# Optimization experiments

Hardware: AMD Instinct MI355X
Metric: run time of the kernel (lower is better)

## Reference

```python
import jax, jax.numpy as jnp
import numpy as np

B, N, M = 2, 1024, 512
D, H, DH = 1024, 16, 64          # features, heads, head dim (D == H*DH)
MID = H * DH
DC = 768                          # context_features
MULT = 4
EPS = 1e-5


def _ln(x, w, b):
    mu = jnp.mean(x, -1, keepdims=True)
    var = jnp.mean((x - mu) ** 2, -1, keepdims=True)
    return (x - mu) * jax.lax.rsqrt(var + EPS) * w + b


def _sincos(n, d):
    inv = 1.0 / (10000.0 ** (jnp.arange(0, d, 2, dtype=jnp.float32) / d))
    ang = jnp.arange(n, dtype=jnp.float32)[:, None] * inv[None, :]
    return jnp.sin(ang), jnp.cos(ang)


def _rope(x, sin, cos):
    # x: [B,H,N,DH]; sin/cos: [N, DH//2]; interleaved even/odd rotation
    s = sin[None, None]
    c = cos[None, None]
    xe = x[..., ::2]
    xo = x[..., 1::2]
    re = xe * c - xo * s
    ro = xe * s + xo * c
    return jnp.stack((re, ro), axis=-1).reshape(x.shape)


def _heads(t):
    b, n, _ = t.shape
    return t.reshape(b, n, H, DH).transpose(0, 2, 1, 3)


def _attn(xq, ctx, wq, wkv, wo, bo):
    q = _heads(xq @ wq)
    k, v = jnp.split(ctx @ wkv, 2, axis=-1)
    k = _heads(k)
    v = _heads(v)
    sq, cq = _sincos(q.shape[2], DH)
    sk, ck = _sincos(k.shape[2], DH)
    q = _rope(q, sq, cq)
    k = _rope(k, sk, ck)
    sim = jnp.einsum('bhnd,bhmd->bhnm', q, k) * (DH ** -0.5)
    a = jax.nn.softmax(sim, axis=-1)
    o = jnp.einsum('bhnm,bhmd->bhnd', a, v)
    o = o.transpose(0, 2, 1, 3).reshape(xq.shape[0], xq.shape[1], MID)
    return o @ wo + bo


def _adaln(x, c, lw, lb, gw, gb, bw, bb):
    g = (c @ gw + gb)[:, None, :]
    bt = (c @ bw + bb)[:, None, :]
    return _ln(x, lw, lb) * (1.0 + g) + bt


def setup_inputs() -> dict:
    ks = jax.random.split(jax.random.key(0), 24)
    s = 0.02
    inp = {
        'x': jax.random.normal(ks[0], (B, N, D), jnp.float32),
        'cond': jax.random.normal(ks[1], (B, D), jnp.float32),
        'context': jax.random.normal(ks[2], (B, M, DC), jnp.float32),
        # AdaLN (attn_mod) — reused for self- and cross-attention pre-norm
        'ln1_w': jnp.ones((D,), jnp.float32),
        'ln1_b': jnp.zeros((D,), jnp.float32),
        'g1_w': jax.random.normal(ks[3], (D, D), jnp.float32) * s,
        'g1_b': jnp.zeros((D,), jnp.float32),
        'b1_w': jax.random.normal(ks[4], (D, D), jnp.float32) * s,
        'b1_b': jnp.zeros((D,), jnp.float32),
        # AdaLN (ffn_mod)
        'ln2_w': jnp.ones((D,), jnp.float32),
        'ln2_b': jnp.zeros((D,), jnp.float32),
        'g2_w': jax.random.normal(ks[5], (D, D), jnp.float32) * s,
        'g2_b': jnp.zeros((D,), jnp.float32),
        'b2_w': jax.random.normal(ks[6], (D, D), jnp.float32) * s,
        'b2_b': jnp.zeros((D,), jnp.float32),
        # self-attention
        'sa_wq': jax.random.normal(ks[7], (D, MID), jnp.float32) * s,
        'sa_wkv': jax.random.normal(ks[8], (D, 2 * MID), jnp.float32) * s,
        'sa_wo': jax.random.normal(ks[9], (MID, D), jnp.float32) * s,
        'sa_bo': jnp.zeros((D,), jnp.float32),
        # cross-attention (context LayerNorm + projections)
        'ca_lnc_w': jnp.ones((DC,), jnp.float32),
        'ca_lnc_b': jnp.zeros((DC,), jnp.float32),
        'ca_wq': jax.random.normal(ks[10], (D, MID), jnp.float32) * s,
        'ca_wkv': jax.random.normal(ks[11], (DC, 2 * MID), jnp.float32) * s,
        'ca_wo': jax.random.normal(ks[12], (MID, D), jnp.float32) * s,
        'ca_bo': jnp.zeros((D,), jnp.float32),
        # FFN
        'ff_w1': jax.random.normal(ks[13], (D, MULT * D), jnp.float32) * s,
        'ff_b1': jnp.zeros((MULT * D,), jnp.float32),
        'ff_w2': jax.random.normal(ks[14], (MULT * D, D), jnp.float32) * s,
        'ff_b2': jnp.zeros((D,), jnp.float32),
    }
    return inp


def reference(x, cond, context,
              ln1_w, ln1_b, g1_w, g1_b, b1_w, b1_b,
              ln2_w, ln2_b, g2_w, g2_b, b2_w, b2_b,
              sa_wq, sa_wkv, sa_wo, sa_bo,
              ca_lnc_w, ca_lnc_b, ca_wq, ca_wkv, ca_wo, ca_bo,
              ff_w1, ff_b1, ff_w2, ff_b2):
    # self-attention with shared attn_mod AdaLN
    attn_in = _adaln(x, cond, ln1_w, ln1_b, g1_w, g1_b, b1_w, b1_b)
    x = _attn(attn_in, attn_in, sa_wq, sa_wkv, sa_wo, sa_bo) + x
    # cross-attention (attn_mod reused, context LayerNorm applied)
    cross_in = _adaln(x, cond, ln1_w, ln1_b, g1_w, g1_b, b1_w, b1_b)
    ctx_n = _ln(context, ca_lnc_w, ca_lnc_b)
    x = _attn(cross_in, ctx_n, ca_wq, ca_wkv, ca_wo, ca_bo) + x
    # FFN with ffn_mod AdaLN, exact GELU (torch default)
    ffn_in = _adaln(x, cond, ln2_w, ln2_b, g2_w, g2_b, b2_w, b2_b)
    h = jax.nn.gelu(ffn_in @ ff_w1 + ff_b1, approximate=False)
    x = h @ ff_w2 + ff_b2 + x
    return x
```

## Files before the change

kernel.cpp:

```cpp
#include <hip/hip_runtime.h>
#include <hip/hip_bf16.h>
#include <math.h>


typedef float f32x4 __attribute__((ext_vector_type(4)));
typedef __bf16 bf16x8 __attribute__((ext_vector_type(8)));
typedef __bf16 bf16x4 __attribute__((ext_vector_type(4)));
typedef __bf16 bf16x2 __attribute__((ext_vector_type(2)));

#define DEVI __device__ __forceinline__

DEVI void gload16(const void* g, void* l) {
  __builtin_amdgcn_global_load_lds((const __attribute__((address_space(1))) void*)g,
                                   (__attribute__((address_space(3))) void*)l, 16, 0, 0);
}

DEVI float fast_gelu(float x) {
  float a = fabsf(x) * 0.7071067811865475f;
  float tt = 1.0f / (1.0f + 0.3275911f * a);
  float p = tt * (0.254829592f + tt * (-0.284496736f + tt * (1.421413741f +
            tt * (-1.453152027f + tt * 1.061405429f))));
  float er = 1.0f - p * __expf(-a * a);
  er = (x < 0.f) ? -er : er;
  return 0.5f * x * (1.0f + er);
}

struct WtDesc {
  const float* src[8];
  __bf16* dst[8];
  int K[8], N[8];
  int tstart[9];
};

__global__ __launch_bounds__(256) void prep_kernel(WtDesc d,
                                                   float2* __restrict__ tbl,
                                                   const float* __restrict__ cond,
                                                   const float* __restrict__ g1w,
                                                   const float* __restrict__ b1w,
                                                   const float* __restrict__ g2w,
                                                   const float* __restrict__ b2w,
                                                   float* __restrict__ part) {
  __shared__ float smem[32][33];
  int blk = blockIdx.x;
  int wtend = d.tstart[8];
  if (blk < wtend) {
    int e = 0;
#pragma unroll
    for (int i = 0; i < 7; ++i) e += (blk >= d.tstart[i + 1]) ? 1 : 0;
    int li = blk - d.tstart[e];
    const float* W = d.src[e];
    __bf16* WT = d.dst[e];
    int K = d.K[e], N = d.N[e];
    int ntx = N >> 5;
    int n0 = (li % ntx) * 32, k0 = (li / ntx) * 32;
    int tx = threadIdx.x & 31, ty = threadIdx.x >> 5;
#pragma unroll
    for (int i = 0; i < 4; ++i) {
      int k = ty + i * 8;
      smem[k][tx] = W[(size_t)(k0 + k) * N + n0 + tx];
    }
    __syncthreads();
#pragma unroll
    for (int i = 0; i < 4; ++i) {
      int n = ty + i * 8;
      WT[(size_t)(n0 + n) * K + k0 + tx] = (__bf16)smem[tx][n];
    }
  } else if (blk < wtend + 128) {
    int idx = (blk - wtend) * 256 + threadIdx.x;
    int n = idx >> 5, i = idx & 31;
    float inv = expf(-(float)(2 * i) * (1.0f / 64.0f) * 9.210340371976184f);
    float ang = (float)n * inv;
    tbl[idx] = make_float2(sinf(ang), cosf(ang));
  } else {
    int f = blk - wtend - 128;
    int dchunk = f & 3, b = (f >> 2) & 1, z = f >> 3;
    int mat = z >> 3, ks = z & 7;
    const float* W = (mat == 0) ? g1w : (mat == 1) ? b1w : (mat == 2) ? g2w : b2w;
    float* sc = &smem[0][0];
    if (threadIdx.x < 128) sc[threadIdx.x] = cond[b * 1024 + ks * 128 + threadIdx.x];
    __syncthreads();
    int dd = dchunk * 256 + threadIdx.x;
    const float* Wp = W + (size_t)(ks * 128) * 1024 + dd;
    float acc = 0.f;
#pragma unroll 8
    for (int k = 0; k < 128; ++k) acc += sc[k] * Wp[(size_t)k * 1024];
    part[(size_t)(z * 2 + b) * 1024 + dd] = acc;
  }
}

__global__ __launch_bounds__(256) void mod_reduce_kernel(
    const float* __restrict__ part,
    const float* __restrict__ g1b, const float* __restrict__ b1b,
    const float* __restrict__ g2b, const float* __restrict__ b2b,
    float* __restrict__ mods) {
  int idx = blockIdx.x * 256 + threadIdx.x;
  int mat = idx >> 11, b = (idx >> 10) & 1, d = idx & 1023;
  float s = 0.f;
#pragma unroll
  for (int ks = 0; ks < 8; ++ks) s += part[(size_t)((mat * 8 + ks) * 2 + b) * 1024 + d];
  const float* Bv = (mat == 0) ? g1b : (mat == 1) ? b1b : (mat == 2) ? g2b : b2b;
  mods[(size_t)(mat * 2 + b) * 1024 + d] = s + Bv[d];
}

__global__ __launch_bounds__(256) void adaln_kernel(const float* __restrict__ X,
                                                    const float* __restrict__ lnw,
                                                    const float* __restrict__ lnb,
                                                    const float* __restrict__ mods,
                                                    int gi, int bi,
                                                    __bf16* __restrict__ out) {
  __shared__ float red[2][4];
  int row = blockIdx.x;
  int b = row >> 10;
  int t = threadIdx.x;
  const float4 xv = ((const float4*)(X + (size_t)row * 1024))[t];
  float s  = xv.x + xv.y + xv.z + xv.w;
  float s2 = xv.x * xv.x + xv.y * xv.y + xv.z * xv.z + xv.w * xv.w;
  int lane = t & 63, w = t >> 6;
#pragma unroll
  for (int off = 32; off > 0; off >>= 1) {
    s += __shfl_down(s, off);
    s2 += __shfl_down(s2, off);
  }
  if (lane == 0) { red[0][w] = s; red[1][w] = s2; }
  __syncthreads();
  s  = red[0][0] + red[0][1] + red[0][2] + red[0][3];
  s2 = red[1][0] + red[1][1] + red[1][2] + red[1][3];
  float mu = s * (1.0f / 1024.0f);
  float var = s2 * (1.0f / 1024.0f) - mu * mu;
  float rstd = rsqrtf(var + 1e-5f);
  const float4 wv = ((const float4*)lnw)[t];
  const float4 bv = ((const float4*)lnb)[t];
  const float4 gv = ((const float4*)(mods + (size_t)(gi * 2 + b) * 1024))[t];
  const float4 tv = ((const float4*)(mods + (size_t)(bi * 2 + b) * 1024))[t];
  bf16x4 ov;
  ov[0] = (__bf16)(((xv.x - mu) * rstd * wv.x + bv.x) * (1.0f + gv.x) + tv.x);
  ov[1] = (__bf16)(((xv.y - mu) * rstd * wv.y + bv.y) * (1.0f + gv.y) + tv.y);
  ov[2] = (__bf16)(((xv.z - mu) * rstd * wv.z + bv.z) * (1.0f + gv.z) + tv.z);
  ov[3] = (__bf16)(((xv.w - mu) * rstd * wv.w + bv.w) * (1.0f + gv.w) + tv.w);
  *(bf16x4*)(out + (size_t)row * 1024 + t * 4) = ov;
}

__global__ __launch_bounds__(256) void ctxln_kernel(const float* __restrict__ X,
                                                    const float* __restrict__ w,
                                                    const float* __restrict__ bias,
                                                    __bf16* __restrict__ out) {
  __shared__ float red[2][4];
  int row = blockIdx.x;
  int t = threadIdx.x;
  const float* xp = X + (size_t)row * 768;
  float v[3];
  float s = 0.f, s2 = 0.f;
#pragma unroll
  for (int i = 0; i < 3; ++i) {
    v[i] = xp[t + i * 256];
    s += v[i];
    s2 += v[i] * v[i];
  }
  int lane = t & 63, wv_ = t >> 6;
#pragma unroll
  for (int off = 32; off > 0; off >>= 1) {
    s += __shfl_down(s, off);
    s2 += __shfl_down(s2, off);
  }
  if (lane == 0) { red[0][wv_] = s; red[1][wv_] = s2; }
  __syncthreads();
  s  = red[0][0] + red[0][1] + red[0][2] + red[0][3];
  s2 = red[1][0] + red[1][1] + red[1][2] + red[1][3];
  float mu = s * (1.0f / 768.0f);
  float var = s2 * (1.0f / 768.0f) - mu * mu;
  float rstd = rsqrtf(var + 1e-5f);
#pragma unroll
  for (int i = 0; i < 3; ++i) {
    int c = t + i * 256;
    out[(size_t)row * 768 + c] = (__bf16)((v[i] - mu) * rstd * w[c] + bias[c]);
  }
}

__global__ __launch_bounds__(256) void vtb_kernel(const __bf16* __restrict__ Vb,
                                                  __bf16* __restrict__ VT, int Ntok) {
  __shared__ __bf16 tile[64][68];
  int bh = blockIdx.x, nt = blockIdx.y;
  int b = bh >> 4, h = bh & 15;
  int t = threadIdx.x;
  int tx = t & 15, ty = t >> 4;
#pragma unroll
  for (int i = 0; i < 4; ++i) {
    int n = ty + i * 16;
    bf16x4 v = *(const bf16x4*)(Vb + (size_t)(b * Ntok + nt * 64 + n) * 1024 + h * 64 + tx * 4);
#pragma unroll
    for (int j = 0; j < 4; ++j) tile[n][tx * 4 + j] = v[j];
  }
  __syncthreads();
#pragma unroll
  for (int i = 0; i < 4; ++i) {
    int d = ty + i * 16;
    bf16x4 o;
#pragma unroll
    for (int j = 0; j < 4; ++j) o[j] = tile[tx * 4 + j][d];
    *(bf16x4*)(VT + ((size_t)bh * 64 + d) * Ntok + nt * 64 + tx * 4) = o;
  }
}

template <int BM, int BN, int EPI, int DEPTH>
__global__ __launch_bounds__(256) void gemm3(const __bf16* __restrict__ A,
                                             const __bf16* __restrict__ BT,
                                             const float* __restrict__ bias,
                                             const float* __restrict__ res,
                                             void* __restrict__ outv,
                                             int M, int N, int K, int kslices,
                                             const float2* __restrict__ tbl,
                                             __bf16* __restrict__ Qro,
                                             __bf16* __restrict__ Kro,
                                             __bf16* __restrict__ Vbo,
                                             int Ntok) {
  constexpr int MI = BM / 32, NI = BN / 32;
  constexpr int NBUF = DEPTH + 1;
  constexpr int LPT = BM / 64 + BN / 64;
  __shared__ __bf16 sA[NBUF][BM * 32];
  __shared__ __bf16 sB[NBUF][BN * 32];
  const int t = threadIdx.x;
  const int w = t >> 6, lane = t & 63;
  const int lr = lane & 15, lg = lane >> 4;
  const int fxor = (lr >> 1) & 3;
  int nwg = gridDim.x * gridDim.y * gridDim.z;
  int flat = blockIdx.x + gridDim.x * (blockIdx.y + gridDim.y * blockIdx.z);
  flat = (flat & 7) * (nwg >> 3) + (flat >> 3);
  const int bm = flat % gridDim.x;
  int rest = flat / gridDim.x;
  const int bn = rest % gridDim.y;
  const int bz = rest / gridDim.y;
  const int wm = (w >> 1) * (BM / 2), wn = (w & 1) * (BN / 2);
  const int kper = K / kslices;
  const int k0 = bz * kper;
  const int nsteps = kper / 32;
  f32x4 acc[MI][NI] = {};

  auto stage = [&](int buf, int kt) {
#pragma unroll
    for (int i = 0; i < BM / 64; ++i) {
      int e8 = i * 256 + t;
      int row = e8 >> 2, c = e8 & 3;
      int scol = (c ^ ((row >> 1) & 3)) << 3;
      gload16(A + (size_t)(bm * BM + row) * K + kt + scol, &sA[buf][e8 * 8]);
    }
#pragma unroll
    for (int i = 0; i < BN / 64; ++i) {
      int e8 = i * 256 + t;
      int row = e8 >> 2, c = e8 & 3;
      int scol = (c ^ ((row >> 1) & 3)) << 3;
      gload16(BT + (size_t)(bn * BN + row) * K + kt + scol, &sB[buf][e8 * 8]);
    }
  };

  auto compute = [&](int buf) {
    bf16x8 af[MI], bfr[NI];
#pragma unroll
    for (int mi = 0; mi < MI; ++mi)
      af[mi] = *(const bf16x8*)(&sA[buf][(wm + mi * 16 + lr) * 32 + ((lg ^ fxor) << 3)]);
#pragma unroll
    for (int ni = 0; ni < NI; ++ni)
      bfr[ni] = *(const bf16x8*)(&sB[buf][(wn + ni * 16 + lr) * 32 + ((lg ^ fxor) << 3)]);
#pragma unroll
    for (int mi = 0; mi < MI; ++mi)
#pragma unroll
      for (int ni = 0; ni < NI; ++ni)
        acc[mi][ni] = __builtin_amdgcn_mfma_f32_16x16x32_bf16(af[mi], bfr[ni], acc[mi][ni], 0, 0, 0);
  };

#pragma unroll
  for (int i = 0; i < DEPTH; ++i) stage(i, k0 + i * 32);

  int it = 0;
  for (; it < nsteps - (DEPTH - 1); ++it) {
    asm volatile("s_waitcnt vmcnt(%0)" :: "n"((DEPTH - 1) * LPT) : "memory");
    __builtin_amdgcn_s_barrier();
    __builtin_amdgcn_sched_barrier(0);
    if (it + DEPTH < nsteps) stage((it + DEPTH) % NBUF, k0 + (it + DEPTH) * 32);
    compute(it % NBUF);
  }
  asm volatile("s_waitcnt vmcnt(0)" ::: "memory");
  __builtin_amdgcn_s_barrier();
  __builtin_amdgcn_sched_barrier(0);
  for (; it < nsteps; ++it) compute(it % NBUF);

#pragma unroll
  for (int mi = 0; mi < MI; ++mi) {
    int row = bm * BM + wm + mi * 16 + lg * 4;
#pragma unroll
    for (int ni = 0; ni < NI; ++ni) {
      int col = bn * BN + wn + ni * 16 + lr;
#pragma unroll
      for (int r = 0; r < 4; ++r) {
        float v = acc[mi][ni][r];
        int erow = row + r;
        size_t off = (size_t)erow * N + col;
        if (EPI == 0) {
          ((float*)outv)[off] = v;
        } else if (EPI == 1) {
          ((float*)outv)[off] = v + bias[col] + res[off];
        } else if (EPI == 2) {
          ((__bf16*)outv)[off] = (__bf16)fast_gelu(v + bias[col]);
        } else if (EPI == 3) {
          ((float*)outv)[(size_t)bz * M * N + off] = v;
        } else if (EPI == 4) {
          float ov = __shfl_xor(v, 1);
          int b = erow >> 10, n = erow & 1023;
          if (col < 2048) {
            int h = (col >> 6) & 15, dh = col & 63;
            float2 sc = tbl[n * 32 + (dh >> 1)];
            float rv = (lr & 1) ? (ov * sc.x + v * sc.y) : (v * sc.y - ov * sc.x);
            __bf16* dst;
            if (col < 1024) { rv *= 0.125f; dst = Qro; } else dst = Kro;
            dst[((size_t)(b * 16 + h) * Ntok + n) * 64 + dh] = (__bf16)rv;
          } else {
            Vbo[(size_t)erow * 1024 + (col - 2048)] = (__bf16)v;
          }
        }
      }
    }
  }
}

__global__ __launch_bounds__(256) void gemm_cross(const __bf16* __restrict__ Aq,
                                                  const __bf16* __restrict__ Bq,
                                                  const __bf16* __restrict__ Akv,
                                                  const __bf16* __restrict__ Bkv,
                                                  const float2* __restrict__ tbl,
                                                  __bf16* __restrict__ Qro,
                                                  __bf16* __restrict__ Kro,
                                                  __bf16* __restrict__ Vbo) {
  constexpr int BM = 128, BN = 64, DEPTH = 3, NBUF = 4, LPT = 3;
  constexpr int MI = 4, NI = 2;
  __shared__ __bf16 sA[NBUF][BM * 32];
  __shared__ __bf16 sB[NBUF][BN * 32];
  const int t = threadIdx.x;
  const int w = t >> 6, lane = t & 63;
  const int lr = lane & 15, lg = lane >> 4;
  const int fxor = (lr >> 1) & 3;
  int flat = blockIdx.x;
  flat = (flat & 7) * 64 + (flat >> 3);
  const bool isq = flat < 256;
  const __bf16* A  = isq ? Aq : Akv;
  const __bf16* BT = isq ? Bq : Bkv;
  const int K = isq ? 1024 : 768;
  int lf = isq ? flat : flat - 256;
  const int bm = isq ? (lf & 15) : (lf & 7);
  const int bn = isq ? (lf >> 4) : (lf >> 3);
  const int wm = (w >> 1) * 64, wn = (w & 1) * 32;
  const int nsteps = K >> 5;
  f32x4 acc[MI][NI] = {};

  auto stage = [&](int buf, int kt) {
#pragma unroll
    for (int i = 0; i < 2; ++i) {
      int e8 = i * 256 + t;
      int row = e8 >> 2, c = e8 & 3;
      int scol = (c ^ ((row >> 1) & 3)) << 3;
      gload16(A + (size_t)(bm * BM + row) * K + kt + scol, &sA[buf][e8 * 8]);
    }
    {
      int e8 = t;
      int row = e8 >> 2, c = e8 & 3;
      int scol = (c ^ ((row >> 1) & 3)) << 3;
      gload16(BT + (size_t)(bn * BN + row) * K + kt + scol, &sB[buf][e8 * 8]);
    }
  };

  auto compute = [&](int buf) {
    bf16x8 af[MI], bfr[NI];
#pragma unroll
    for (int mi = 0; mi < MI; ++mi)
      af[mi] = *(const bf16x8*)(&sA[buf][(wm + mi * 16 + lr) * 32 + ((lg ^ fxor) << 3)]);
#pragma unroll
    for (int ni = 0; ni < NI; ++ni)
      bfr[ni] = *(const bf16x8*)(&sB[buf][(wn + ni * 16 + lr) * 32 + ((lg ^ fxor) << 3)]);
#pragma unroll
    for (int mi = 0; mi < MI; ++mi)
#pragma unroll
      for (int ni = 0; ni < NI; ++ni)
        acc[mi][ni] = __builtin_amdgcn_mfma_f32_16x16x32_bf16(af[mi], bfr[ni], acc[mi][ni], 0, 0, 0);
  };

#pragma unroll
  for (int i = 0; i < DEPTH; ++i) stage(i, i * 32);

  int it = 0;
  for (; it < nsteps - (DEPTH - 1); ++it) {
    asm volatile("s_waitcnt vmcnt(%0)" :: "n"((DEPTH - 1) * LPT) : "memory");
    __builtin_amdgcn_s_barrier();
    __builtin_amdgcn_sched_barrier(0);
    if (it + DEPTH < nsteps) stage((it + DEPTH) % NBUF, (it + DEPTH) * 32);
    compute(it % NBUF);
  }
  asm volatile("s_waitcnt vmcnt(0)" ::: "memory");
  __builtin_amdgcn_s_barrier();
  __builtin_amdgcn_sched_barrier(0);
  for (; it < nsteps; ++it) compute(it % NBUF);

#pragma unroll
  for (int mi = 0; mi < MI; ++mi) {
    int row = bm * 128 + wm + mi * 16 + lg * 4;
#pragma unroll
    for (int ni = 0; ni < NI; ++ni) {
      int col = bn * 64 + wn + ni * 16 + lr;
#pragma unroll
      for (int r = 0; r < 4; ++r) {
        float v = acc[mi][ni][r];
        int erow = row + r;
        float ov = __shfl_xor(v, 1);
        if (isq) {
          int b = erow >> 10, n = erow & 1023;
          int h = col >> 6, dh = col & 63;
          float2 sc = tbl[n * 32 + (dh >> 1)];
          float rv = ((lr & 1) ? (ov * sc.x + v * sc.y) : (v * sc.y - ov * sc.x)) * 0.125f;
          Qro[((size_t)(b * 16 + h) * 1024 + n) * 64 + dh] = (__bf16)rv;
        } else {
          int b = erow >> 9, n = erow & 511;
          if (col < 1024) {
            int h = col >> 6, dh = col & 63;
            float2 sc = tbl[n * 32 + (dh >> 1)];
            float rv = (lr & 1) ? (ov * sc.x + v * sc.y) : (v * sc.y - ov * sc.x);
            Kro[((size_t)(b * 16 + h) * 512 + n) * 64 + dh] = (__bf16)rv;
          } else {
            Vbo[(size_t)erow * 1024 + (col - 1024)] = (__bf16)v;
          }
        }
      }
    }
  }
}

__global__ __launch_bounds__(256) void ff2red_kernel(const float* __restrict__ part,
                                                     const float* __restrict__ bias,
                                                     const float* __restrict__ res,
                                                     float* __restrict__ out, int MN, int N) {
  int idx = blockIdx.x * 256 + threadIdx.x;
  float4 p0 = ((const float4*)part)[idx];
  float4 p1 = ((const float4*)(part + MN))[idx];
  float4 rr = ((const float4*)res)[idx];
  int colb = (idx * 4) & (N - 1);
  float4 bb = *(const float4*)(bias + colb);
  float4 o;
  o.x = p0.x + p1.x + bb.x + rr.x;
  o.y = p0.y + p1.y + bb.y + rr.y;
  o.z = p0.z + p1.z + bb.z + rr.z;
  o.w = p0.w + p1.w + bb.w + rr.w;
  ((float4*)out)[idx] = o;
}

template <int KITERS>
__global__ __launch_bounds__(256) void attn_kernel(const __bf16* __restrict__ Qr,
                                                   const __bf16* __restrict__ Kr,
                                                   const __bf16* __restrict__ VT,
                                                   __bf16* __restrict__ O,
                                                   int Nq, int Nk) {
  __shared__ __bf16 sK[2][64 * 64];
  __shared__ __bf16 sV[2][64 * 64];
  __shared__ __bf16 Pl[4][16 * 64];
  const int t = threadIdx.x, w = t >> 6, lane = t & 63;
  const int lr = lane & 15, lg = lane >> 4;
  const int lsrc = lane & 48;
  const int swz = (lr & 7) << 3;
  int flat = blockIdx.x + (blockIdx.y << 4);
  flat = (flat & 7) * 64 + (flat >> 3);
  const int bh = flat >> 4;
  const int q0 = (flat & 15) * 64 + w * 16;
  const int b = bh >> 4, h = bh & 15;

  auto stage = [&](int buf, int kt) {
#pragma unroll
    for (int i = 0; i < 2; ++i) {
      int e8 = i * 256 + t;
      int row = e8 >> 3, col8 = e8 & 7;
      int scol = (col8 ^ (row & 7)) << 3;
      gload16(Kr + ((size_t)bh * Nk + kt + row) * 64 + scol, &sK[buf][e8 * 8]);
      gload16(VT + ((size_t)bh * 64 + row) * Nk + kt + scol, &sV[buf][e8 * 8]);
    }
  };

  bf16x8 qf[2];
#pragma unroll
  for (int kh = 0; kh < 2; ++kh)
    qf[kh] = *(const bf16x8*)(Qr + ((size_t)bh * Nq + q0 + lr) * 64 + kh * 32 + lg * 8);
  f32x4 accO[4] = {};
  float m = -INFINITY, l = 0.f;

  stage(0, 0);
  __syncthreads();
  int cur = 0;
#pragma unroll
  for (int it = 0; it < KITERS; ++it) {
    if (it + 1 < KITERS) stage(cur ^ 1, (it + 1) * 64);
    f32x4 s[4] = {};
#pragma unroll
    for (int nf = 0; nf < 4; ++nf) {
      int r = nf * 16 + lr;
#pragma unroll
      for (int kh = 0; kh < 2; ++kh) {
        bf16x8 kf = *(const bf16x8*)(&sK[cur][r * 64 + (((kh * 4 + lg) ^ (lr & 7)) << 3)]);
        s[nf] = __builtin_amdgcn_mfma_f32_16x16x32_bf16(kf, qf[kh], s[nf], 0, 0, 0);
      }
    }
    float p[16];
#pragma unroll
    for (int j = 0; j < 16; ++j) p[j] = s[j >> 2][j & 3];
    float pm = p[0];
#pragma unroll
    for (int j = 1; j < 16; ++j) pm = fmaxf(pm, p[j]);
    pm = fmaxf(pm, __shfl_xor(pm, 16));
    pm = fmaxf(pm, __shfl_xor(pm, 32));
    if (!__all(pm <= m + 8.f)) {
      float mnew = fmaxf(m, pm);
      float resc = __expf(m - mnew);
      float rq[4];
#pragma unroll
      for (int r = 0; r < 4; ++r) rq[r] = __shfl(resc, lsrc | (lg * 4 + r));
#pragma unroll
      for (int df = 0; df < 4; ++df)
#pragma unroll
        for (int r = 0; r < 4; ++r) accO[df][r] *= rq[r];
      l *= resc;
      m = mnew;
    }
    float rs = 0.f;
#pragma unroll
    for (int j = 0; j < 16; ++j) { p[j] = __expf(p[j] - m); rs += p[j]; }
    rs += __shfl_xor(rs, 16);
    rs += __shfl_xor(rs, 32);
    l += rs;
#pragma unroll
    for (int nf = 0; nf < 4; ++nf)
#pragma unroll
      for (int jj = 0; jj < 2; ++jj) {
        int k = nf * 16 + lg * 4 + 2 * jj;
        bf16x2 pk;
        pk[0] = (__bf16)p[nf * 4 + 2 * jj];
        pk[1] = (__bf16)p[nf * 4 + 2 * jj + 1];
        *(bf16x2*)(&Pl[w][lr * 64 + (k ^ swz)]) = pk;
      }
    bf16x8 pa0 = *(const bf16x8*)(&Pl[w][lr * 64 + ((lg * 8) ^ swz)]);
    bf16x8 pa1 = *(const bf16x8*)(&Pl[w][lr * 64 + ((32 + lg * 8) ^ swz)]);
#pragma unroll
    for (int df = 0; df < 4; ++df) {
      int d = df * 16 + lr;
      bf16x8 vf0 = *(const bf16x8*)(&sV[cur][d * 64 + ((lg ^ (lr & 7)) << 3)]);
      bf16x8 vf1 = *(const bf16x8*)(&sV[cur][d * 64 + (((4 + lg) ^ (lr & 7)) << 3)]);
      accO[df] = __builtin_amdgcn_mfma_f32_16x16x32_bf16(pa0, vf0, accO[df], 0, 0, 0);
      accO[df] = __builtin_amdgcn_mfma_f32_16x16x32_bf16(pa1, vf1, accO[df], 0, 0, 0);
    }
    __syncthreads();
    cur ^= 1;
  }
  float lq[4];
#pragma unroll
  for (int r = 0; r < 4; ++r) lq[r] = __shfl(l, lsrc | (lg * 4 + r));
#pragma unroll
  for (int r = 0; r < 4; ++r) {
    float inv = 1.0f / lq[r];
    int n = q0 + lg * 4 + r;
#pragma unroll
    for (int df = 0; df < 4; ++df)
      O[(size_t)(b * 1024 + n) * 1024 + h * 64 + df * 16 + lr] = (__bf16)(accO[df][r] * inv);
  }
}

extern "C" void kernel_launch(void* const* d_in, const int* in_sizes, int n_in,
                              void* d_out, int out_size, void* d_ws, size_t ws_size,
                              hipStream_t stream) {
  (void)in_sizes; (void)n_in; (void)out_size; (void)ws_size;
  const float* x       = (const float*)d_in[0];
  const float* cond    = (const float*)d_in[1];
  const float* ctx     = (const float*)d_in[2];
  const float* ln1_w   = (const float*)d_in[3];
  const float* ln1_b   = (const float*)d_in[4];
  const float* g1_w    = (const float*)d_in[5];
  const float* g1_b    = (const float*)d_in[6];
  const float* b1_w    = (const float*)d_in[7];
  const float* b1_b    = (const float*)d_in[8];
  const float* ln2_w   = (const float*)d_in[9];
  const float* ln2_b   = (const float*)d_in[10];
  const float* g2_w    = (const float*)d_in[11];
  const float* g2_b    = (const float*)d_in[12];
  const float* b2_w    = (const float*)d_in[13];
  const float* b2_b    = (const float*)d_in[14];
  const float* sa_wq   = (const float*)d_in[15];
  const float* sa_wkv  = (const float*)d_in[16];
  const float* sa_wo   = (const float*)d_in[17];
  const float* sa_bo   = (const float*)d_in[18];
  const float* ca_lnc_w = (const float*)d_in[19];
  const float* ca_lnc_b = (const float*)d_in[20];
  const float* ca_wq   = (const float*)d_in[21];
  const float* ca_wkv  = (const float*)d_in[22];
  const float* ca_wo   = (const float*)d_in[23];
  const float* ca_bo   = (const float*)d_in[24];
  const float* ff_w1   = (const float*)d_in[25];
  const float* ff_b1   = (const float*)d_in[26];
  const float* ff_w2   = (const float*)d_in[27];
  const float* ff_b2   = (const float*)d_in[28];
  float* out = (float*)d_out;

  char* ws = (char*)d_ws;
  size_t o = 0;
  auto alloc = [&](size_t bytes) {
    void* p = ws + o;
    o += (bytes + 255) & ~(size_t)255;
    return p;
  };

  __bf16* wqT   = (__bf16*)alloc(1024ull * 1024 * 2);
  __bf16* wkvT  = (__bf16*)alloc(2048ull * 1024 * 2);
  __bf16* woT   = (__bf16*)alloc(1024ull * 1024 * 2);
  __bf16* cwqT  = (__bf16*)alloc(1024ull * 1024 * 2);
  __bf16* cwkvT = (__bf16*)alloc(2048ull * 768 * 2);
  __bf16* cwoT  = (__bf16*)alloc(1024ull * 1024 * 2);
  __bf16* ff1T  = (__bf16*)alloc(4096ull * 1024 * 2);
  __bf16* ff2T  = (__bf16*)alloc(1024ull * 4096 * 2);
  float*  mods  = (float*)alloc(4ull * 2 * 1024 * 4);
  float2* tbl   = (float2*)alloc(1024ull * 32 * 8);
  __bf16* ain   = (__bf16*)alloc(2048ull * 1024 * 2);
  float*  Qf    = (float*)alloc(2048ull * 1024 * 4);
  float*  KVf   = (float*)alloc(2048ull * 2048 * 4);
  __bf16* ctxn  = (__bf16*)alloc(1024ull * 768 * 2);
  __bf16* Qr    = (__bf16*)alloc(2048ull * 1024 * 2);
  __bf16* Kr    = (__bf16*)alloc(2048ull * 1024 * 2);
  __bf16* VTb   = (__bf16*)alloc(2048ull * 1024 * 2);
  __bf16* Ob    = (__bf16*)alloc(2048ull * 1024 * 2);
  float*  x1    = (float*)alloc(2048ull * 1024 * 4);
  float*  x2    = (float*)alloc(2048ull * 1024 * 4);
  __bf16* hb    = (__bf16*)KVf;
  float*  pbuf  = (float*)Qr;
  float*  wopb  = (float*)KVf;
  float*  mpart = (float*)Qf;
  __bf16* Vb    = (__bf16*)Qf;

  WtDesc wd;
  const float* srcs[8] = {sa_wq, sa_wkv, sa_wo, ca_wq, ca_wkv, ca_wo, ff_w1, ff_w2};
  __bf16* dsts[8] = {wqT, wkvT, woT, cwqT, cwkvT, cwoT, ff1T, ff2T};
  int Ks[8] = {1024, 1024, 1024, 1024, 768, 1024, 1024, 4096};
  int Ns[8] = {1024, 2048, 1024, 1024, 2048, 1024, 4096, 1024};
  int cum = 0;
  for (int i = 0; i < 8; ++i) {
    wd.src[i] = srcs[i]; wd.dst[i] = dsts[i]; wd.K[i] = Ks[i]; wd.N[i] = Ns[i];
    wd.tstart[i] = cum;
    cum += (Ks[i] >> 5) * (Ns[i] >> 5);
  }
  wd.tstart[8] = cum;
  prep_kernel<<<cum + 128 + 256, 256, 0, stream>>>(wd, tbl, cond, g1_w, b1_w, g2_w, b2_w, mpart);
  mod_reduce_kernel<<<32, 256, 0, stream>>>(mpart, g1_b, b1_b, g2_b, b2_b, mods);

  adaln_kernel<<<2048, 256, 0, stream>>>(x, ln1_w, ln1_b, mods, 0, 1, ain);
  gemm3<128, 64, 4, 3><<<dim3(16, 48), 256, 0, stream>>>(ain, wqT, nullptr, nullptr, nullptr,
                                                         2048, 3072, 1024, 1, tbl, Qr, Kr, Vb, 1024);
  vtb_kernel<<<dim3(32, 16), 256, 0, stream>>>(Vb, VTb, 1024);
  attn_kernel<16><<<dim3(16, 32), 256, 0, stream>>>(Qr, Kr, VTb, Ob, 1024, 1024);
  gemm3<128, 64, 3, 3><<<dim3(16, 16, 2), 256, 0, stream>>>(Ob, woT, nullptr, nullptr, wopb,
                                                            2048, 1024, 1024, 2, nullptr, nullptr, nullptr, nullptr, 0);
  ff2red_kernel<<<2048, 256, 0, stream>>>(wopb, sa_bo, x, x1, 2048 * 1024, 1024);

  adaln_kernel<<<2048, 256, 0, stream>>>(x1, ln1_w, ln1_b, mods, 0, 1, ain);
  ctxln_kernel<<<1024, 256, 0, stream>>>(ctx, ca_lnc_w, ca_lnc_b, ctxn);
  gemm_cross<<<512, 256, 0, stream>>>(ain, cwqT, ctxn, cwkvT, tbl, Qr, Kr, Vb);
  vtb_kernel<<<dim3(32, 8), 256, 0, stream>>>(Vb, VTb, 512);
  attn_kernel<8><<<dim3(16, 32), 256, 0, stream>>>(Qr, Kr, VTb, Ob, 1024, 512);
  gemm3<128, 64, 3, 3><<<dim3(16, 16, 2), 256, 0, stream>>>(Ob, cwoT, nullptr, nullptr, wopb,
                                                            2048, 1024, 1024, 2, nullptr, nullptr, nullptr, nullptr, 0);
  ff2red_kernel<<<2048, 256, 0, stream>>>(wopb, ca_bo, x1, x2, 2048 * 1024, 1024);

  adaln_kernel<<<2048, 256, 0, stream>>>(x2, ln2_w, ln2_b, mods, 2, 3, ain);
  gemm3<128, 128, 2, 2><<<dim3(16, 32), 256, 0, stream>>>(ain, ff1T, ff_b1, nullptr, hb,
                                                          2048, 4096, 1024, 1, nullptr, nullptr, nullptr, nullptr, 0);
  gemm3<128, 64, 3, 3><<<dim3(16, 16, 2), 256, 0, stream>>>(hb, ff2T, nullptr, nullptr, pbuf,
                                                            2048, 1024, 4096, 2, nullptr, nullptr, nullptr, nullptr, 0);
  ff2red_kernel<<<2048, 256, 0, stream>>>(pbuf, ff_b2, x2, out, 2048 * 1024, 1024);
}
```

Baseline: 246.4 us.

## Fuse split-K reduction with AdaLN and widen weight-transpose tiles

Replaces the split-K reduce plus residual kernel followed by a separate AdaLN kernel with one kernel. The fused kernel sums the partials, adds bias and residual, writes the new residual stream, then applies LayerNorm and modulation from registers, so the residual is not read back from memory. The weight transpose/bf16 conversion in the prep kernel now handles 32x128 tiles with float4 loads and 16-byte bf16x8 stores, which cuts the block count and uses wider memory transactions. Both changes save memory traffic and launches, at the cost of more LDS per prep block.

```diff
diff --git a/kernel.cpp b/kernel.cpp
--- a/kernel.cpp
+++ b/kernel.cpp
@@ -40,9 +40,10 @@
                                                    const float* __restrict__ g2w,
                                                    const float* __restrict__ b2w,
                                                    float* __restrict__ part) {
-  __shared__ float smem[32][33];
+  __shared__ float smem[32 * 129];
   int blk = blockIdx.x;
   int wtend = d.tstart[8];
+  int t = threadIdx.x;
   if (blk < wtend) {
     int e = 0;
 #pragma unroll
@@ -51,22 +52,28 @@
     const float* W = d.src[e];
     __bf16* WT = d.dst[e];
     int K = d.K[e], N = d.N[e];
-    int ntx = N >> 5;
-    int n0 = (li % ntx) * 32, k0 = (li / ntx) * 32;
-    int tx = threadIdx.x & 31, ty = threadIdx.x >> 5;
+    int ntx = N >> 7;
+    int n0 = (li % ntx) * 128, k0 = (li / ntx) * 32;
+    int tx = t & 31, ty = t >> 5;
 #pragma unroll
     for (int i = 0; i < 4; ++i) {
       int k = ty + i * 8;
-      smem[k][tx] = W[(size_t)(k0 + k) * N + n0 + tx];
+      f32x4 v = *(const f32x4*)(W + (size_t)(k0 + k) * N + n0 + tx * 4);
+#pragma unroll
+      for (int j = 0; j < 4; ++j) smem[k * 129 + tx * 4 + j] = v[j];
     }
     __syncthreads();
-#pragma unroll
-    for (int i = 0; i < 4; ++i) {
-      int n = ty + i * 8;
-      WT[(size_t)(n0 + n) * K + k0 + tx] = (__bf16)smem[tx][n];
+    int kc = t & 3;
+#pragma unroll
+    for (int i = 0; i < 2; ++i) {
+      int n = i * 64 + (t >> 2);
+      bf16x8 o;
+#pragma unroll
+      for (int j = 0; j < 8; ++j) o[j] = (__bf16)smem[(kc * 8 + j) * 129 + n];
+      *(bf16x8*)(WT + (size_t)(n0 + n) * K + k0 + kc * 8) = o;
     }
   } else if (blk < wtend + 128) {
-    int idx = (blk - wtend) * 256 + threadIdx.x;
+    int idx = (blk - wtend) * 256 + t;
     int n = idx >> 5, i = idx & 31;
     float inv = expf(-(float)(2 * i) * (1.0f / 64.0f) * 9.210340371976184f);
     float ang = (float)n * inv;
@@ -76,10 +83,10 @@
     int dchunk = f & 3, b = (f >> 2) & 1, z = f >> 3;
     int mat = z >> 3, ks = z & 7;
     const float* W = (mat == 0) ? g1w : (mat == 1) ? b1w : (mat == 2) ? g2w : b2w;
-    float* sc = &smem[0][0];
-    if (threadIdx.x < 128) sc[threadIdx.x] = cond[b * 1024 + ks * 128 + threadIdx.x];
+    float* sc = smem;
+    if (t < 128) sc[t] = cond[b * 1024 + ks * 128 + t];
     __syncthreads();
-    int dd = dchunk * 256 + threadIdx.x;
+    int dd = dchunk * 256 + t;
     const float* Wp = W + (size_t)(ks * 128) * 1024 + dd;
     float acc = 0.f;
 #pragma unroll 8
@@ -138,6 +145,57 @@
   ov[2] = (__bf16)(((xv.z - mu) * rstd * wv.z + bv.z) * (1.0f + gv.z) + tv.z);
   ov[3] = (__bf16)(((xv.w - mu) * rstd * wv.w + bv.w) * (1.0f + gv.w) + tv.w);
   *(bf16x4*)(out + (size_t)row * 1024 + t * 4) = ov;
+}
+
+__global__ __launch_bounds__(256) void red_adaln_kernel(const float* __restrict__ part,
+                                                        const float* __restrict__ bias,
+                                                        const float* __restrict__ res,
+                                                        const float* __restrict__ lnw,
+                                                        const float* __restrict__ lnb,
+                                                        const float* __restrict__ mods,
+                                                        int gi, int bi, int MN,
+                                                        float* __restrict__ xout,
+                                                        __bf16* __restrict__ ain) {
+  __shared__ float red[2][4];
+  int row = blockIdx.x;
+  int b = row >> 10;
+  int t = threadIdx.x;
+  size_t base = (size_t)row * 1024 + t * 4;
+  float4 p0 = *(const float4*)(part + base);
+  float4 p1 = *(const float4*)(part + MN + base);
+  float4 rr = *(const float4*)(res + base);
+  float4 bb = ((const float4*)bias)[t];
+  float4 y;
+  y.x = p0.x + p1.x + bb.x + rr.x;
+  y.y = p0.y + p1.y + bb.y + rr.y;
+  y.z = p0.z + p1.z + bb.z + rr.z;
+  y.w = p0.w + p1.w + bb.w + rr.w;
+  *(float4*)(xout + base) = y;
+  float s  = y.x + y.y + y.z + y.w;
+  float s2 = y.x * y.x + y.y * y.y + y.z * y.z + y.w * y.w;
+  int lane = t & 63, w = t >> 6;
+#pragma unroll
+  for (int off = 32; off > 0; off >>= 1) {
+    s += __shfl_down(s, off);
+    s2 += __shfl_down(s2, off);
+  }
+  if (lane == 0) { red[0][w] = s; red[1][w] = s2; }
+  __syncthreads();
+  s  = red[0][0] + red[0][1] + red[0][2] + red[0][3];
+  s2 = red[1][0] + red[1][1] + red[1][2] + red[1][3];
+  float mu = s * (1.0f / 1024.0f);
+  float var = s2 * (1.0f / 1024.0f) - mu * mu;
+  float rstd = rsqrtf(var + 1e-5f);
+  const float4 wv = ((const float4*)lnw)[t];
+  const float4 bv = ((const float4*)lnb)[t];
+  const float4 gv = ((const float4*)(mods + (size_t)(gi * 2 + b) * 1024))[t];
+  const float4 tv = ((const float4*)(mods + (size_t)(bi * 2 + b) * 1024))[t];
+  bf16x4 ov;
+  ov[0] = (__bf16)(((y.x - mu) * rstd * wv.x + bv.x) * (1.0f + gv.x) + tv.x);
+  ov[1] = (__bf16)(((y.y - mu) * rstd * wv.y + bv.y) * (1.0f + gv.y) + tv.y);
+  ov[2] = (__bf16)(((y.z - mu) * rstd * wv.z + bv.z) * (1.0f + gv.z) + tv.z);
+  ov[3] = (__bf16)(((y.w - mu) * rstd * wv.w + bv.w) * (1.0f + gv.w) + tv.w);
+  *(bf16x4*)(ain + (size_t)row * 1024 + t * 4) = ov;
 }
 
 __global__ __launch_bounds__(256) void ctxln_kernel(const float* __restrict__ X,
@@ -642,7 +700,7 @@
   for (int i = 0; i < 8; ++i) {
     wd.src[i] = srcs[i]; wd.dst[i] = dsts[i]; wd.K[i] = Ks[i]; wd.N[i] = Ns[i];
     wd.tstart[i] = cum;
-    cum += (Ks[i] >> 5) * (Ns[i] >> 5);
+    cum += (Ks[i] >> 5) * (Ns[i] >> 7);
   }
   wd.tstart[8] = cum;
   prep_kernel<<<cum + 128 + 256, 256, 0, stream>>>(wd, tbl, cond, g1_w, b1_w, g2_w, b2_w, mpart);
@@ -655,18 +713,18 @@
   attn_kernel<16><<<dim3(16, 32), 256, 0, stream>>>(Qr, Kr, VTb, Ob, 1024, 1024);
   gemm3<128, 64, 3, 3><<<dim3(16, 16, 2), 256, 0, stream>>>(Ob, woT, nullptr, nullptr, wopb,
                                                             2048, 1024, 1024, 2, nullptr, nullptr, nullptr, nullptr, 0);
-  ff2red_kernel<<<2048, 256, 0, stream>>>(wopb, sa_bo, x, x1, 2048 * 1024, 1024);
-
-  adaln_kernel<<<2048, 256, 0, stream>>>(x1, ln1_w, ln1_b, mods, 0, 1, ain);
+  red_adaln_kernel<<<2048, 256, 0, stream>>>(wopb, sa_bo, x, ln1_w, ln1_b, mods, 0, 1,
+                                             2048 * 1024, x1, ain);
+
   ctxln_kernel<<<1024, 256, 0, stream>>>(ctx, ca_lnc_w, ca_lnc_b, ctxn);
   gemm_cross<<<512, 256, 0, stream>>>(ain, cwqT, ctxn, cwkvT, tbl, Qr, Kr, Vb);
   vtb_kernel<<<dim3(32, 8), 256, 0, stream>>>(Vb, VTb, 512);
   attn_kernel<8><<<dim3(16, 32), 256, 0, stream>>>(Qr, Kr, VTb, Ob, 1024, 512);
   gemm3<128, 64, 3, 3><<<dim3(16, 16, 2), 256, 0, stream>>>(Ob, cwoT, nullptr, nullptr, wopb,
                                                             2048, 1024, 1024, 2, nullptr, nullptr, nullptr, nullptr, 0);
-  ff2red_kernel<<<2048, 256, 0, stream>>>(wopb, ca_bo, x1, x2, 2048 * 1024, 1024);
-
-  adaln_kernel<<<2048, 256, 0, stream>>>(x2, ln2_w, ln2_b, mods, 2, 3, ain);
+  red_adaln_kernel<<<2048, 256, 0, stream>>>(wopb, ca_bo, x1, ln2_w, ln2_b, mods, 2, 3,
+                                             2048 * 1024, x2, ain);
+
   gemm3<128, 128, 2, 2><<<dim3(16, 32), 256, 0, stream>>>(ain, ff1T, ff_b1, nullptr, hb,
                                                           2048, 4096, 1024, 1, nullptr, nullptr, nullptr, nullptr, 0);
   gemm3<128, 64, 3, 3><<<dim3(16, 16, 2), 256, 0, stream>>>(hb, ff2T, nullptr, nullptr, pbuf,
```

After: 241.5 us, median of 2. 1.02x faster.
